# Kernel tuning notes

Hardware: AMD Instinct MI355X
Metric: run time of the kernel (lower is better)

The kernel has to match this reference:

```python
import jax, jax.numpy as jnp
import numpy as np

VOCAB, EBD, ATT_H, R, T, IMG_C = 50257, 512, 512, 196, 1024, 512


def setup_inputs() -> dict:
    key = jax.random.key(0)
    ks = jax.random.split(key, 10)
    question = jax.random.randint(ks[0], (T,), 0, VOCAB)
    img_feat = jax.random.normal(ks[1], (R, IMG_C), dtype=jnp.float32)
    emb_table = (jax.random.normal(ks[2], (VOCAB, EBD), dtype=jnp.float32) * 0.02).at[0].set(0.0)  # padding_idx=0
    W_img = jax.random.normal(ks[3], (EBD, IMG_C), dtype=jnp.float32) * (1.0 / np.sqrt(IMG_C))
    b_img = jnp.zeros((EBD,), dtype=jnp.float32)
    W_ai = jax.random.normal(ks[4], (ATT_H, EBD), dtype=jnp.float32) * (1.0 / np.sqrt(EBD))  # att_img, no bias
    W_aw = jax.random.normal(ks[5], (ATT_H, EBD), dtype=jnp.float32) * (1.0 / np.sqrt(EBD))  # att_word
    b_aw = jnp.zeros((ATT_H,), dtype=jnp.float32)
    w_att = jax.random.normal(ks[6], (ATT_H,), dtype=jnp.float32) * (1.0 / np.sqrt(ATT_H))  # att -> scalar
    b_att = jnp.zeros((), dtype=jnp.float32)
    return {"question": question, "img_feat": img_feat, "emb_table": emb_table,
            "W_img": W_img, "b_img": b_img, "W_ai": W_ai, "W_aw": W_aw,
            "b_aw": b_aw, "w_att": w_att, "b_att": b_att}


def reference(question, img_feat, emb_table, W_img, b_img, W_ai, W_aw, b_aw, w_att, b_att):
    # img_feature = relu(Linear(512 -> ebd)(vgg_regions));  [R, EBD]
    img = jax.nn.relu(img_feat @ W_img.T + b_img)
    # per-word embeddings  [T, EBD]
    E = emb_table[question]
    # additive attention: tanh(attImg[r] + attWord[t]) . w_att + b_att  -> [T, R]
    AI = img @ W_ai.T                       # [R, H]
    AW = E @ W_aw.T + b_aw                  # [T, H]
    scores = jnp.einsum('trh,h->tr', jnp.tanh(AI[None, :, :] + AW[:, None, :]), w_att) + b_att
    w = jax.nn.softmax(scores, axis=-1)     # softmax over regions, [T, R]
    # weighted sum of img features, divided by n_regions (faithful to original)
    ctx = (w @ img) / img.shape[0]          # [T, EBD]
    # attedInput: concat(new_img_feature, word_emd)  [T, 2*EBD]
    return jnp.concatenate([ctx, E], axis=-1)
```

## Files before the change

### kernel.cpp

```cpp
#include <hip/hip_runtime.h>

#define PRESCALE 2.8853900817779268f

typedef short s16;
typedef unsigned short u16;
typedef unsigned int u32;
typedef __attribute__((ext_vector_type(8))) short short8v;
typedef __attribute__((ext_vector_type(4))) float f4;

#if __has_builtin(__builtin_amdgcn_exp2f)
#define EXP2(x) __builtin_amdgcn_exp2f(x)
#else
static __device__ inline float exp2_raw(float x){ float r; asm("v_exp_f32 %0, %1":"=v"(r):"v"(x)); return r; }
#define EXP2(x) exp2_raw(x)
#endif
#if __has_builtin(__builtin_amdgcn_rcpf)
#define RCP(x) __builtin_amdgcn_rcpf(x)
#else
static __device__ inline float rcp_raw(float x){ float r; asm("v_rcp_f32 %0, %1":"=v"(r):"v"(x)); return r; }
#define RCP(x) rcp_raw(x)
#endif

__device__ inline u16 f2bf(float f){
  union{u32 i; float f;} v; v.f = f;
  u32 r = v.i + 0x7fffu + ((v.i >> 16) & 1u);
  return (u16)(r >> 16);
}

__global__ __launch_bounds__(256) void k_prep(
    const float* __restrict__ W_img, const float* __restrict__ W_ai,
    const float* __restrict__ W_aw,  const float* __restrict__ img_feat,
    const int* __restrict__ question, const float* __restrict__ emb,
    s16* __restrict__ Wb, s16* __restrict__ Xb, s16* __restrict__ Eb,
    float* __restrict__ out){
  for (int g = blockIdx.x*256 + threadIdx.x; g < 360448; g += gridDim.x*256){
    if (g < 196608){
      const int i = g*4, w = i >> 18;
      const float sc = (w == 0) ? 1.f : PRESCALE;
      const float* src = (w==0) ? W_img : ((w==1) ? W_ai : W_aw);
      float4 v = *reinterpret_cast<const float4*>(src + (i & 262143));
      ushort4 o; o.x=f2bf(v.x*sc); o.y=f2bf(v.y*sc); o.z=f2bf(v.z*sc); o.w=f2bf(v.w*sc);
      *reinterpret_cast<ushort4*>(Wb + i) = o;
    } else if (g < 229376){
      const int i = (g - 196608)*4;
      ushort4 o = make_ushort4(0,0,0,0);
      if ((i >> 9) < 196){
        float4 v = *reinterpret_cast<const float4*>(img_feat + i);
        o.x=f2bf(v.x); o.y=f2bf(v.y); o.z=f2bf(v.z); o.w=f2bf(v.w);
      }
      *reinterpret_cast<ushort4*>(Xb + i) = o;
    } else {
      const int i = (g - 229376)*4;
      const int t = i >> 9, c = i & 511;
      float4 v = *reinterpret_cast<const float4*>(emb + (size_t)question[t]*512 + c);
      *reinterpret_cast<float4*>(out + (size_t)t*1024 + 512 + c) = v;
      ushort4 o; o.x=f2bf(v.x); o.y=f2bf(v.y); o.z=f2bf(v.z); o.w=f2bf(v.w);
      *reinterpret_cast<ushort4*>(Eb + i) = o;
    }
  }
}

__device__ inline void mfma_core(const s16* __restrict__ A, const s16* __restrict__ B,
                                 int m0, int n0, int lr, int lg, f4 acc[2][2]){
  const s16* pa0 = A + (size_t)(m0 + lr)*512 + lg*8;
  const s16* pa1 = pa0 + 16*512;
  const s16* pb0 = B + (size_t)(n0 + lr)*512 + lg*8;
  const s16* pb1 = pb0 + 16*512;
  #pragma unroll 4
  for (int k = 0; k < 512; k += 32){
    short8v a0 = *reinterpret_cast<const short8v*>(pa0 + k);
    short8v a1 = *reinterpret_cast<const short8v*>(pa1 + k);
    short8v b0 = *reinterpret_cast<const short8v*>(pb0 + k);
    short8v b1 = *reinterpret_cast<const short8v*>(pb1 + k);
    acc[0][0] = __builtin_amdgcn_mfma_f32_16x16x32_bf16(a0, b0, acc[0][0], 0, 0, 0);
    acc[0][1] = __builtin_amdgcn_mfma_f32_16x16x32_bf16(a0, b1, acc[0][1], 0, 0, 0);
    acc[1][0] = __builtin_amdgcn_mfma_f32_16x16x32_bf16(a1, b0, acc[1][0], 0, 0, 0);
    acc[1][1] = __builtin_amdgcn_mfma_f32_16x16x32_bf16(a1, b1, acc[1][1], 0, 0, 0);
  }
}

__global__ __launch_bounds__(256) void k_gemms(
    const s16* __restrict__ Xb, const s16* __restrict__ Wb_img,
    const s16* __restrict__ Wb_aw, const s16* __restrict__ Eb,
    const float* __restrict__ b_img, const float* __restrict__ b_aw,
    float* __restrict__ img, s16* __restrict__ img_b,
    float* __restrict__ AWT4){
  const int tid = threadIdx.x, w = tid>>6, l = tid&63;
  const int lr = l & 15, lg = l >> 4;
  f4 acc[2][2] = {};
  if (blockIdx.x < 32){
    const int m0 = (blockIdx.x >> 3)*64 + (w>>1)*32;
    const int n0 = (blockIdx.x & 7)*64 + (w&1)*32;
    mfma_core(Xb, Wb_img, m0, n0, lr, lg, acc);
    #pragma unroll
    for (int i = 0; i < 2; ++i){
      #pragma unroll
      for (int j = 0; j < 2; ++j){
        const int nn = n0 + j*16 + lr;
        const float bc = b_img[nn];
        #pragma unroll
        for (int p = 0; p < 4; ++p){
          const int mm = m0 + i*16 + lg*4 + p;
          float v = fmaxf(acc[i][j][p] + bc, 0.f);
          img[(size_t)mm*512 + nn] = v;
          img_b[(size_t)mm*512 + nn] = (s16)f2bf(v);
        }
      }
    }
  } else {
    const int blk = blockIdx.x - 32;
    const int m0 = (blk >> 4)*64 + (w>>1)*32;
    const int n0 = (blk & 15)*64 + (w&1)*32;
    mfma_core(Wb_aw, Eb, m0, n0, lr, lg, acc);
    #pragma unroll
    for (int i = 0; i < 2; ++i){
      const int mb = m0 + i*16 + lg*4;
      #pragma unroll
      for (int j = 0; j < 2; ++j){
        const int nn = n0 + j*16 + lr;
        f4 o;
        #pragma unroll
        for (int p = 0; p < 4; ++p)
          o[p] = acc[i][j][p] + b_aw[mb+p]*PRESCALE;
        *reinterpret_cast<f4*>(AWT4 + (size_t)(mb>>2)*4096 + nn*4) = o;
      }
    }
  }
}

__global__ __launch_bounds__(256) void k_ai(
    const s16* __restrict__ img_b, const s16* __restrict__ Wb_ai,
    float* __restrict__ AI){
  const int tid = threadIdx.x, w = tid>>6, l = tid&63;
  const int lr = l & 15, lg = l >> 4;
  const int m0 = (blockIdx.x >> 3)*64 + (w>>1)*32;
  const int n0 = (blockIdx.x & 7)*64 + (w&1)*32;
  f4 acc[2][2] = {};
  mfma_core(img_b, Wb_ai, m0, n0, lr, lg, acc);
  #pragma unroll
  for (int i = 0; i < 2; ++i)
    #pragma unroll
    for (int j = 0; j < 2; ++j){
      const int nn = n0 + j*16 + lr;
      #pragma unroll
      for (int p = 0; p < 4; ++p){
        const int mm = m0 + i*16 + lg*4 + p;
        AI[(size_t)mm*512 + nn] = acc[i][j][p];
      }
    }
}

__global__ __launch_bounds__(512) void k_score(
    const float* __restrict__ AI, const float* __restrict__ AWT4,
    const float* __restrict__ w_att, float* __restrict__ ST){
  __shared__ float ais[16*512 + 512];
  float* wsh = ais + 16*512;
  const int tid = threadIdx.x, w = tid>>6, l = tid&63;
  const int rq = blockIdx.x >> 4, tq = blockIdx.x & 15;
  {
    const f4* src = reinterpret_cast<const f4*>(AI + (size_t)rq*16*512);
    f4* dst = reinterpret_cast<f4*>(ais);
    #pragma unroll
    for (int i = 0; i < 4; ++i) dst[tid + i*512] = src[tid + i*512];
    if (tid < 128)
      reinterpret_cast<f4*>(wsh)[tid] = reinterpret_cast<const f4*>(w_att)[tid];
  }
  __syncthreads();
  const float* a0 = ais + (size_t)(w*2)*512;
  const float* a1 = a0 + 512;
  const int t = tq*64 + l;
  const float* ap = AWT4 + (size_t)t*4;
  float s0=0.f, s1=0.f, s2=0.f, s3=0.f;
  #pragma unroll 8
  for (int hg = 0; hg < 128; ++hg){
    f4 x  = *reinterpret_cast<const f4*>(ap + (size_t)hg*4096);
    f4 av = *reinterpret_cast<const f4*>(a0 + hg*4);
    f4 bv = *reinterpret_cast<const f4*>(a1 + hg*4);
    f4 wv = *reinterpret_cast<const f4*>(wsh + hg*4);
    s0 += wv.x*RCP(EXP2(av.x+x.x)+1.f) + wv.y*RCP(EXP2(av.y+x.y)+1.f);
    s1 += wv.z*RCP(EXP2(av.z+x.z)+1.f) + wv.w*RCP(EXP2(av.w+x.w)+1.f);
    s2 += wv.x*RCP(EXP2(bv.x+x.x)+1.f) + wv.y*RCP(EXP2(bv.y+x.y)+1.f);
    s3 += wv.z*RCP(EXP2(bv.z+x.z)+1.f) + wv.w*RCP(EXP2(bv.w+x.w)+1.f);
  }
  const int r = rq*16 + w*2;
  ST[(size_t)r*1024 + t]     = s0+s1;
  ST[(size_t)(r+1)*1024 + t] = s2+s3;
}

__global__ __launch_bounds__(256) void k_ctx(
    const float* __restrict__ ST, const float* __restrict__ img,
    float* __restrict__ out){
  __shared__ float wgt[196][16];
  __shared__ float red[16][16];
  const int tid = threadIdx.x;
  const int t0 = blockIdx.x*16, e0 = blockIdx.y*64;
  const int rs = tid>>4, tl = tid&15;

  float m = 1e30f;
  for (int k = 0; k < 13; ++k){
    const int r = rs + 16*k;
    if (r < 196) m = fminf(m, ST[(size_t)r*1024 + t0 + tl]);
  }
  red[rs][tl] = m;
  __syncthreads();
  if (tid < 16){
    float mm = red[0][tid];
    #pragma unroll
    for (int i = 1; i < 16; ++i) mm = fminf(mm, red[i][tid]);
    red[0][tid] = mm;
  }
  __syncthreads();
  const float mt = red[0][tl];
  float sum = 0.f;
  for (int k = 0; k < 13; ++k){
    const int r = rs + 16*k;
    if (r < 196){
      float p = EXP2(PRESCALE*(mt - ST[(size_t)r*1024 + t0 + tl]));
      wgt[r][tl] = p;
      sum += p;
    }
  }
  __syncthreads();
  red[rs][tl] = sum;
  __syncthreads();
  if (tid < 16){
    float ss = 0.f;
    #pragma unroll
    for (int i = 0; i < 16; ++i) ss += red[i][tid];
    red[0][tid] = 1.f / (ss * 196.f);
  }
  __syncthreads();
  const float inv = red[0][tl];
  for (int k = 0; k < 13; ++k){
    const int r = rs + 16*k;
    if (r < 196) wgt[r][tl] *= inv;
  }
  __syncthreads();

  const int e = e0 + (tid & 63), tq = tid >> 6;
  float acc[4] = {0.f, 0.f, 0.f, 0.f};
  const float* ip = img + e;
  #pragma unroll 4
  for (int r = 0; r < 196; ++r){
    const float f = ip[(size_t)r*512];
    float4 w4 = *reinterpret_cast<const float4*>(&wgt[r][tq*4]);
    acc[0] += w4.x*f; acc[1] += w4.y*f; acc[2] += w4.z*f; acc[3] += w4.w*f;
  }
  #pragma unroll
  for (int j = 0; j < 4; ++j)
    out[(size_t)(t0 + tq*4 + j)*1024 + e] = acc[j];
}

extern "C" void kernel_launch(void* const* d_in, const int* in_sizes, int n_in,
                              void* d_out, int out_size, void* d_ws, size_t ws_size,
                              hipStream_t stream) {
  const int*   question = (const int*)d_in[0];
  const float* img_feat = (const float*)d_in[1];
  const float* emb      = (const float*)d_in[2];
  const float* W_img    = (const float*)d_in[3];
  const float* b_img    = (const float*)d_in[4];
  const float* W_ai     = (const float*)d_in[5];
  const float* W_aw     = (const float*)d_in[6];
  const float* b_aw     = (const float*)d_in[7];
  const float* w_att    = (const float*)d_in[8];
  float* out = (float*)d_out;

  char* ws = (char*)d_ws;
  s16*   Wb    = (s16*)(ws);
  s16*   Xb    = (s16*)(ws + 1572864);
  s16*   Eb    = (s16*)(ws + 1835008);
  float* img   = (float*)(ws + 2883584);
  s16*   img_b = (s16*)(ws + 3407872);
  float* AI    = (float*)(ws + 3670016);
  float* AWT4  = (float*)(ws + 4194304);
  float* ST    = (float*)(ws + 6291456);

  hipLaunchKernelGGL(k_prep,  dim3(512),   dim3(256), 0, stream,
                     W_img, W_ai, W_aw, img_feat, question, emb, Wb, Xb, Eb, out);
  hipLaunchKernelGGL(k_gemms, dim3(160),   dim3(256), 0, stream,
                     Xb, Wb, Wb + 2*262144, Eb, b_img, b_aw, img, img_b, AWT4);
  hipLaunchKernelGGL(k_ai,    dim3(32),    dim3(256), 0, stream,
                     img_b, Wb + 262144, AI);
  hipLaunchKernelGGL(k_score, dim3(256),   dim3(512), 0, stream,
                     AI, AWT4, w_att, ST);
  hipLaunchKernelGGL(k_ctx,   dim3(64,8),  dim3(256), 0, stream, ST, img, out);
}
```

Measured before the change: 82.31 us.

## Split score kernel over hidden chunks with register-cached AW and partial-sum reduction

The score kernel is restructured to tile over (5-region blocks, 8 hidden chunks of 64, 2 token halves). Each thread now keeps its 16 AW vectors in registers, reuses them across 5 regions, and writes per-chunk partial scores. k_ctx sums the 8 partials and caches the result in shared memory before the softmax. This raises grid parallelism from 256 to 640 blocks and cuts repeated AW global loads, at the cost of an 8x larger partial-score buffer that k_ctx must read. The larger buffer may also extend past the previous workspace allocation.

```diff
diff --git a/kernel.cpp b/kernel.cpp
--- a/kernel.cpp
+++ b/kernel.cpp
@@ -150,45 +150,52 @@
     }
 }
 
+#define RB5 5
 __global__ __launch_bounds__(512) void k_score(
     const float* __restrict__ AI, const float* __restrict__ AWT4,
-    const float* __restrict__ w_att, float* __restrict__ ST){
-  __shared__ float ais[16*512 + 512];
-  float* wsh = ais + 16*512;
+    const float* __restrict__ w_att, float* __restrict__ STp){
+  __shared__ float ais[RB5][64];
+  __shared__ float wsh[64];
   const int tid = threadIdx.x, w = tid>>6, l = tid&63;
-  const int rq = blockIdx.x >> 4, tq = blockIdx.x & 15;
-  {
-    const f4* src = reinterpret_cast<const f4*>(AI + (size_t)rq*16*512);
-    f4* dst = reinterpret_cast<f4*>(ais);
-    #pragma unroll
-    for (int i = 0; i < 4; ++i) dst[tid + i*512] = src[tid + i*512];
-    if (tid < 128)
-      reinterpret_cast<f4*>(wsh)[tid] = reinterpret_cast<const f4*>(w_att)[tid];
-  }
-  __syncthreads();
-  const float* a0 = ais + (size_t)(w*2)*512;
-  const float* a1 = a0 + 512;
-  const int t = tq*64 + l;
-  const float* ap = AWT4 + (size_t)t*4;
-  float s0=0.f, s1=0.f, s2=0.f, s3=0.f;
-  #pragma unroll 8
-  for (int hg = 0; hg < 128; ++hg){
-    f4 x  = *reinterpret_cast<const f4*>(ap + (size_t)hg*4096);
-    f4 av = *reinterpret_cast<const f4*>(a0 + hg*4);
-    f4 bv = *reinterpret_cast<const f4*>(a1 + hg*4);
-    f4 wv = *reinterpret_cast<const f4*>(wsh + hg*4);
-    s0 += wv.x*RCP(EXP2(av.x+x.x)+1.f) + wv.y*RCP(EXP2(av.y+x.y)+1.f);
-    s1 += wv.z*RCP(EXP2(av.z+x.z)+1.f) + wv.w*RCP(EXP2(av.w+x.w)+1.f);
-    s2 += wv.x*RCP(EXP2(bv.x+x.x)+1.f) + wv.y*RCP(EXP2(bv.y+x.y)+1.f);
-    s3 += wv.z*RCP(EXP2(bv.z+x.z)+1.f) + wv.w*RCP(EXP2(bv.w+x.w)+1.f);
-  }
-  const int r = rq*16 + w*2;
-  ST[(size_t)r*1024 + t]     = s0+s1;
-  ST[(size_t)(r+1)*1024 + t] = s2+s3;
+  const int rr = blockIdx.x, hc = blockIdx.y, th = blockIdx.z;
+  const int r0 = rr*RB5, h0 = hc*64;
+  if (tid < 80){
+    const int i = tid >> 4, j = tid & 15;
+    const int r = min(r0 + i, 195);
+    *reinterpret_cast<f4*>(&ais[i][j*4]) =
+        *reinterpret_cast<const f4*>(AI + (size_t)r*512 + h0 + j*4);
+  } else if (tid < 96){
+    const int j = tid - 80;
+    *reinterpret_cast<f4*>(&wsh[j*4]) =
+        *reinterpret_cast<const f4*>(w_att + h0 + j*4);
+  }
+  const int t = th*512 + w*64 + l;
+  const int hg0 = hc*16;
+  f4 awr[16];
+  #pragma unroll
+  for (int j = 0; j < 16; ++j)
+    awr[j] = *reinterpret_cast<const f4*>(AWT4 + (size_t)(hg0+j)*4096 + t*4);
+  __syncthreads();
+  #pragma unroll
+  for (int i = 0; i < RB5; ++i){
+    const int r = r0 + i;
+    if (r >= 196) break;
+    float a0=0.f, a1=0.f, a2=0.f, a3=0.f;
+    #pragma unroll
+    for (int j = 0; j < 16; ++j){
+      f4 av = *reinterpret_cast<const f4*>(&ais[i][j*4]);
+      f4 wv = *reinterpret_cast<const f4*>(&wsh[j*4]);
+      a0 += wv.x*RCP(EXP2(av.x+awr[j].x)+1.f);
+      a1 += wv.y*RCP(EXP2(av.y+awr[j].y)+1.f);
+      a2 += wv.z*RCP(EXP2(av.z+awr[j].z)+1.f);
+      a3 += wv.w*RCP(EXP2(av.w+awr[j].w)+1.f);
+    }
+    STp[((size_t)hc<<18) + (size_t)r*1024 + t] = (a0+a1)+(a2+a3);
+  }
 }
 
 __global__ __launch_bounds__(256) void k_ctx(
-    const float* __restrict__ ST, const float* __restrict__ img,
+    const float* __restrict__ STp, const float* __restrict__ img,
     float* __restrict__ out){
   __shared__ float wgt[196][16];
   __shared__ float red[16][16];
@@ -199,7 +206,14 @@
   float m = 1e30f;
   for (int k = 0; k < 13; ++k){
     const int r = rs + 16*k;
-    if (r < 196) m = fminf(m, ST[(size_t)r*1024 + t0 + tl]);
+    if (r < 196){
+      float s = 0.f;
+      #pragma unroll
+      for (int c = 0; c < 8; ++c)
+        s += STp[((size_t)c<<18) + (size_t)r*1024 + t0 + tl];
+      wgt[r][tl] = s;
+      m = fminf(m, s);
+    }
   }
   red[rs][tl] = m;
   __syncthreads();
@@ -215,7 +229,7 @@
   for (int k = 0; k < 13; ++k){
     const int r = rs + 16*k;
     if (r < 196){
-      float p = EXP2(PRESCALE*(mt - ST[(size_t)r*1024 + t0 + tl]));
+      float p = EXP2(PRESCALE*(mt - wgt[r][tl]));
       wgt[r][tl] = p;
       sum += p;
     }
@@ -273,15 +287,15 @@
   s16*   img_b = (s16*)(ws + 3407872);
   float* AI    = (float*)(ws + 3670016);
   float* AWT4  = (float*)(ws + 4194304);
-  float* ST    = (float*)(ws + 6291456);
-
-  hipLaunchKernelGGL(k_prep,  dim3(512),   dim3(256), 0, stream,
+  float* STp   = (float*)(ws + 6291456);
+
+  hipLaunchKernelGGL(k_prep,  dim3(512),    dim3(256), 0, stream,
                      W_img, W_ai, W_aw, img_feat, question, emb, Wb, Xb, Eb, out);
-  hipLaunchKernelGGL(k_gemms, dim3(160),   dim3(256), 0, stream,
+  hipLaunchKernelGGL(k_gemms, dim3(160),    dim3(256), 0, stream,
                      Xb, Wb, Wb + 2*262144, Eb, b_img, b_aw, img, img_b, AWT4);
-  hipLaunchKernelGGL(k_ai,    dim3(32),    dim3(256), 0, stream,
+  hipLaunchKernelGGL(k_ai,    dim3(32),     dim3(256), 0, stream,
                      img_b, Wb + 262144, AI);
-  hipLaunchKernelGGL(k_score, dim3(256),   dim3(512), 0, stream,
-                     AI, AWT4, w_att, ST);
-  hipLaunchKernelGGL(k_ctx,   dim3(64,8),  dim3(256), 0, stream, ST, img, out);
-}
+  hipLaunchKernelGGL(k_score, dim3(40,8,2), dim3(512), 0, stream,
+                     AI, AWT4, w_att, STp);
+  hipLaunchKernelGGL(k_ctx,   dim3(64,8),   dim3(256), 0, stream, STp, img, out);
+}
```

Result: faster. 79.88 us (-3.0%).
